# Kernel optimization log

Hardware: AMD Instinct MI355X
Metric: run time of the kernel (lower is better)

Reference implementation:

```python
import jax, jax.numpy as jnp
import numpy as np

N = 16384          # num nodes
E = 262144         # num edges (before self loops)
IN_DIM = 128
HID = 128
OUT = 2
TRIM = 0.1
MAX_DEG = 48       # padded max in-degree (incl. self loop); safe bound for Poisson(16)+1
BN_EPS = 1e-5


def _lin_params(key, fan_in, fan_out):
    kw, kb = jax.random.split(key)
    s = 1.0 / np.sqrt(fan_in)
    W = jax.random.uniform(kw, (fan_in, fan_out), jnp.float32, -s, s)
    b = jax.random.uniform(kb, (fan_out,), jnp.float32, -s, s)
    return W, b


def setup_inputs() -> dict:
    key = jax.random.key(0)
    ks = jax.random.split(key, 8)
    x = jax.random.normal(ks[0], (N, IN_DIM), jnp.float32)
    edge_index = jax.random.randint(ks[1], (2, E), 0, N, jnp.int32)
    Wl0, bl0 = _lin_params(ks[2], IN_DIM, HID)
    Wr0, br0 = _lin_params(ks[3], IN_DIM, HID)
    Wl1, bl1 = _lin_params(ks[4], HID, HID)
    Wr1, br1 = _lin_params(ks[5], HID, HID)
    Wl2, bl2 = _lin_params(ks[6], HID, OUT)
    Wr2, br2 = _lin_params(ks[7], HID, OUT)
    g0 = jnp.ones((HID,), jnp.float32); be0 = jnp.zeros((HID,), jnp.float32)
    g1 = jnp.ones((HID,), jnp.float32); be1 = jnp.zeros((HID,), jnp.float32)
    return dict(x=x, edge_index=edge_index,
                Wl0=Wl0, bl0=bl0, Wr0=Wr0, br0=br0, g0=g0, be0=be0,
                Wl1=Wl1, bl1=bl1, Wr1=Wr1, br1=br1, g1=g1, be1=be1,
                Wl2=Wl2, bl2=bl2, Wr2=Wr2, br2=br2)


def _forward(edge_index, x, Wl0, bl0, Wr0, br0, g0, be0,
             Wl1, bl1, Wr1, br1, g1, be1, Wl2, bl2, Wr2, br2):
    loops = jnp.arange(N, dtype=edge_index.dtype)
    row = jnp.concatenate([edge_index[0], loops])   # source nodes
    col = jnp.concatenate([edge_index[1], loops])   # destination nodes
    counts = jax.ops.segment_sum(jnp.ones_like(col), col, num_segments=N)  # in-degree, int
    deg = jnp.maximum(counts, 1).astype(x.dtype)
    norm = 1.0 / deg[col]                            # 1/deg(dst), per edge

    # Edge ordering grouped by destination node; rank = slot within the node's group.
    perm = jnp.argsort(col, stable=True)
    col_s = col[perm]
    starts = jnp.cumsum(counts) - counts
    rank = jnp.arange(col.shape[0], dtype=counts.dtype) - starts[col_s]
    node_id = jnp.where(rank < MAX_DEG, col_s, N)    # overflow slots -> OOB, dropped by scatter

    t = jnp.maximum(1, jnp.floor(counts.astype(jnp.float32) * TRIM).astype(counts.dtype))
    tcnt = counts - 2 * t
    pos = jnp.arange(MAX_DEG)[None, :]
    sel = (pos >= t[:, None]) & (pos < (counts - t)[:, None])   # [N, MAX_DEG]
    use_trim = (counts >= 5) & (tcnt > 0)
    inv_tcnt = 1.0 / jnp.maximum(tcnt, 1).astype(x.dtype)

    def trimmed_scatter(msg):
        # plain mean fallback
        mean = jax.ops.segment_sum(msg, col, num_segments=N) / deg[:, None]
        d = msg.shape[1]
        # padded per-node buffer; +inf pads sort to the end (never selected by `sel`)
        dense = jnp.full((N, MAX_DEG, d), jnp.inf, msg.dtype)
        dense = dense.at[node_id, rank].set(msg[perm], mode='drop')
        sdense = jnp.sort(dense, axis=1)             # per-feature sort within each node
        tmean = jnp.sum(jnp.where(sel[:, :, None], sdense, 0.0), axis=1) * inv_tcnt[:, None]
        return jnp.where(use_trim[:, None], tmean, mean)

    def conv(h, Wl, bl, Wr, br):
        msg = (h @ Wl + bl)[row] * norm[:, None]
        return trimmed_scatter(msg) + h @ Wr + br

    bn_scale = jnp.float32(1.0 / np.sqrt(1.0 + BN_EPS))  # eval-mode BN: running mean 0, var 1
    h = conv(x, Wl0, bl0, Wr0, br0)
    h = jax.nn.relu(h * bn_scale * g0 + be0)
    h = conv(h, Wl1, bl1, Wr1, br1)
    h = jax.nn.relu(h * bn_scale * g1 + be1)
    return conv(h, Wl2, bl2, Wr2, br2)


def reference(x, edge_index, Wl0, bl0, Wr0, br0, g0, be0,
              Wl1, bl1, Wr1, br1, g1, be1, Wl2, bl2, Wr2, br2):
    return _forward(edge_index, x, Wl0, bl0, Wr0, br0, g0, be0,
                    Wl1, bl1, Wr1, br1, g1, be1, Wl2, bl2, Wr2, br2)
```

## Files before the change

### kernel.cpp

```cpp
#include <hip/hip_runtime.h>
#include <hip/hip_fp16.h>
#include <math.h>

#define GN    16384
#define MAXD  48
#define BN_SCALE 0.9999950000374998f

typedef __attribute__((ext_vector_type(8))) short short8;
typedef __attribute__((ext_vector_type(4))) float f32x4;
typedef __attribute__((ext_vector_type(2))) float f32x2v;
typedef __attribute__((ext_vector_type(4))) float f32x4v;
typedef _Float16 __attribute__((ext_vector_type(2))) h2v;

__device__ inline short f2bf(float x) {
    unsigned u = __float_as_uint(x);
    return (short)((u + 0x7fffu + ((u >> 16) & 1u)) >> 16);
}
__device__ inline float bf2f(short s) {
    return __uint_as_float(((unsigned)(unsigned short)s) << 16);
}

struct F2 { float x, y; };
__device__ inline F2 f2min(F2 a, F2 b) { return {fminf(a.x, b.x), fminf(a.y, b.y)}; }
__device__ inline F2 f2max(F2 a, F2 b) { return {fmaxf(a.x, b.x), fmaxf(a.y, b.y)}; }

struct Trk {
    F2 tot, s0, s1, s2, s3, l0, l1, l2, l3;
};
__device__ inline void trk_init(Trk& T) {
    T.tot = {0.f, 0.f};
    T.s0 = T.s1 = T.s2 = T.s3 = { INFINITY,  INFINITY};
    T.l0 = T.l1 = T.l2 = T.l3 = {-INFINITY, -INFINITY};
}
__device__ inline void trk_push_light(Trk& T, F2 x, bool valid) {
    F2 xs = {valid ? x.x :  INFINITY, valid ? x.y :  INFINITY};
    F2 xl = {valid ? x.x : -INFINITY, valid ? x.y : -INFINITY};
    T.tot.x += valid ? x.x : 0.f;
    T.tot.y += valid ? x.y : 0.f;
    T.s0 = f2min(T.s0, xs);
    T.l0 = f2max(T.l0, xl);
}
__device__ inline void trk_push_full(Trk& T, F2 x, bool valid) {
    F2 a = {valid ? x.x :  INFINITY, valid ? x.y :  INFINITY};
    F2 b = {valid ? x.x : -INFINITY, valid ? x.y : -INFINITY};
    T.tot.x += valid ? x.x : 0.f;
    T.tot.y += valid ? x.y : 0.f;
    F2 t0 = f2min(T.s0, a); a = f2max(T.s0, a); T.s0 = t0;
    F2 t1 = f2min(T.s1, a); a = f2max(T.s1, a); T.s1 = t1;
    F2 t2 = f2min(T.s2, a); a = f2max(T.s2, a); T.s2 = t2;
    T.s3 = f2min(T.s3, a);
    F2 u0 = f2max(T.l0, b); b = f2min(T.l0, b); T.l0 = u0;
    F2 u1 = f2max(T.l1, b); b = f2min(T.l1, b); T.l1 = u1;
    F2 u2 = f2max(T.l2, b); b = f2min(T.l2, b); T.l2 = u2;
    T.l3 = f2max(T.l3, b);
}
__device__ inline F2 trk_finish(const Trk& T, int cnt) {
    int t = (int)floorf((float)cnt * 0.1f);
    if (t < 1) t = 1;
    int tcnt = cnt - 2 * t;
    bool use_trim = (cnt >= 5) && (tcnt > 0);
    float dd = (float)cnt;
    F2 res;
    if (use_trim) {
        int tt = min(t, 4);
        F2 bot = T.s0, top = T.l0;
        if (tt > 1) { bot.x += T.s1.x; bot.y += T.s1.y; top.x += T.l1.x; top.y += T.l1.y; }
        if (tt > 2) { bot.x += T.s2.x; bot.y += T.s2.y; top.x += T.l2.x; top.y += T.l2.y; }
        if (tt > 3) { bot.x += T.s3.x; bot.y += T.s3.y; top.x += T.l3.x; top.y += T.l3.y; }
        float inv = 1.0f / (dd * (float)tcnt);
        res.x = (T.tot.x - bot.x - top.x) * inv;
        res.y = (T.tot.y - bot.y - top.y) * inv;
    } else {
        float inv = 1.0f / (dd * dd);
        res.x = T.tot.x * inv;
        res.y = T.tot.y * inv;
    }
    return res;
}

__device__ inline F2 trim_core(const _Float16* __restrict__ HL,
                               const int* __restrict__ srow, int cnt, int d, int f2i)
{
    Trk T; trk_init(T);
    bool light = (cnt < 20);
    for (int i = 0; i < d; i += 8) {
        h2v b[8];
        #pragma unroll
        for (int k = 0; k < 8; ++k) {
            int ia = min(i + k, d - 1);
            b[k] = *reinterpret_cast<const h2v*>(HL + srow[ia] + f2i);
        }
        if (light) {
            #pragma unroll
            for (int k = 0; k < 8; ++k)
                trk_push_light(T, {(float)b[k][0], (float)b[k][1]}, i + k < d);
        } else {
            #pragma unroll
            for (int k = 0; k < 8; ++k)
                trk_push_full(T, {(float)b[k][0], (float)b[k][1]}, i + k < d);
        }
    }
    return trk_finish(T, cnt);
}

__global__ __launch_bounds__(256) void k_prep(
    int* __restrict__ fill,
    const float* __restrict__ Wl0, const float* __restrict__ Wr0,
    const float* __restrict__ Wl1, const float* __restrict__ Wr1,
    short* __restrict__ W5)
{
    int t = blockIdx.x * 256 + threadIdx.x;
    fill[t] = 0;

    int layer = t >> 13;
    int g     = t & 8191;
    int split = (g >> 12) & 1;
    int ks    = (g >> 10) & 3;
    int nt    = (g >> 6) & 15;
    int l     = g & 63;
    int q = l >> 4, r = l & 15;
    int n = nt * 16 + r;
    const float* W = (n < 128) ? (layer ? Wl1 : Wl0) : (layer ? Wr1 : Wr0);
    int ncol = n & 127;
    short8 o8;
    #pragma unroll
    for (int j = 0; j < 8; ++j) {
        int k = ks * 32 + (j >> 2) * 16 + q * 4 + (j & 3);
        float wv = W[k * 128 + ncol];
        short hi = f2bf(wv);
        o8[j] = split ? f2bf(wv - bf2f(hi)) : hi;
    }
    *reinterpret_cast<short8*>(W5 + ((size_t)layer * 8192 + g) * 8) = o8;
}

template<int NT>
__device__ inline void gemm_tile_t(const short8 Ahi[4], const short8 Alo[4],
                                   const short* __restrict__ W5,
                                   const float* __restrict__ bl,
                                   const float* __restrict__ br,
                                   _Float16* __restrict__ HL, float* __restrict__ HR,
                                   int tile, int half, int ntg0, int q, int r, int l)
{
    f32x4 acc[NT];
    #pragma unroll
    for (int nt = 0; nt < NT; ++nt) {
        int ntg = ntg0 + nt;
        float b = (ntg < 8) ? bl[ntg * 16 + r] : br[(ntg - 8) * 16 + r];
        acc[nt] = (f32x4){b, b, b, b};
    }
    #pragma unroll
    for (int ks = 0; ks < 4; ++ks) {
        #pragma unroll
        for (int nt = 0; nt < NT; ++nt) {
            int ntg = ntg0 + nt;
            short8 Bhi = *reinterpret_cast<const short8*>(
                W5 + ((size_t)(ks * 16 + ntg) * 64 + l) * 8);
            short8 Blo = *reinterpret_cast<const short8*>(
                W5 + ((size_t)((4 + ks) * 16 + ntg) * 64 + l) * 8);
            acc[nt] = __builtin_amdgcn_mfma_f32_16x16x32_bf16(Ahi[ks], Bhi, acc[nt], 0, 0, 0);
            acc[nt] = __builtin_amdgcn_mfma_f32_16x16x32_bf16(Ahi[ks], Blo, acc[nt], 0, 0, 0);
            acc[nt] = __builtin_amdgcn_mfma_f32_16x16x32_bf16(Alo[ks], Bhi, acc[nt], 0, 0, 0);
        }
    }
    const int rb = tile * 32 + half * 16 + 4 * q;
    #pragma unroll
    for (int nt = 0; nt < NT; ++nt) {
        int ntg = ntg0 + nt;
        if (ntg < 8) {
            int c = ntg * 16 + r;
            #pragma unroll
            for (int j = 0; j < 4; ++j)
                HL[(size_t)(rb + j) * 128 + c] = (_Float16)acc[nt][j];
        } else {
            int c = (ntg - 8) * 16 + r;
            #pragma unroll
            for (int j = 0; j < 4; ++j)
                __builtin_nontemporal_store(acc[nt][j], &HR[(size_t)(rb + j) * 128 + c]);
        }
    }
}

__global__ __launch_bounds__(512, 4) void k_fused0(
    const float* __restrict__ X, const int* __restrict__ ei, int E,
    int* __restrict__ adj, int* __restrict__ fill,
    const short* __restrict__ W5,
    const float* __restrict__ bl, const float* __restrict__ br,
    _Float16* __restrict__ HL, float* __restrict__ HR)
{
    const int tid = threadIdx.x;
    if (blockIdx.x >= 512) {
        const int* src = ei;
        const int* dst = ei + E;
        int g0 = (blockIdx.x - 512) * 512 + tid;
        for (int i = g0; i < E + GN; i += 64 * 512) {
            int s, dv;
            if (i < E) { s = src[i]; dv = dst[i]; }
            else       { s = i - E;  dv = i - E; }
            int slot = atomicAdd(&fill[dv], 1);
            if (slot < MAXD) adj[dv * MAXD + slot] = s;
        }
        return;
    }
    const int w = tid >> 6, l = tid & 63;
    const int q = l >> 4, r = l & 15;
    const int half = w & 1, quarter = w >> 1;
    const int rowA = blockIdx.x * 32 + half * 16 + r;

    short8 Ahi[4], Alo[4];
    const f32x4v* xp = reinterpret_cast<const f32x4v*>(X + (size_t)rowA * 128);
    #pragma unroll
    for (int h = 0; h < 8; ++h) {
        f32x4v v = __builtin_nontemporal_load(xp + h * 4 + q);
        float xv[4] = {v.x, v.y, v.z, v.w};
        int ks = h >> 1, hk = h & 1;
        #pragma unroll
        for (int j = 0; j < 4; ++j) {
            short hi = f2bf(xv[j]);
            Ahi[ks][hk * 4 + j] = hi;
            Alo[ks][hk * 4 + j] = f2bf(xv[j] - bf2f(hi));
        }
    }
    gemm_tile_t<4>(Ahi, Alo, W5, bl, br, HL, HR, blockIdx.x, half, quarter * 4, q, r, l);
}

__global__ __launch_bounds__(512, 4) void k_fused1(
    const _Float16* __restrict__ HL0, const float* __restrict__ HR0,
    const int* __restrict__ adj, const int* __restrict__ fill,
    const float* __restrict__ g, const float* __restrict__ be,
    const short* __restrict__ W5,
    const float* __restrict__ bl, const float* __restrict__ br,
    _Float16* __restrict__ HL1, float* __restrict__ HR1)
{
    __shared__ float hbs[32][132];
    __shared__ int sadj[8][2][MAXD];
    const int tid = threadIdx.x, w = tid >> 6, l = tid & 63;
    const int f2i = l * 2;
    const int v0 = blockIdx.x * 32;
    const float gs0 = BN_SCALE * g[f2i], gs1 = BN_SCALE * g[f2i + 1];
    const float be0 = be[f2i], be1 = be[f2i + 1];

    for (int p = 0; p < 2; ++p) {
        const int vA = v0 + w * 4 + p * 2;
        const int vB = vA + 1;
        const int cA = fill[vA], cB = fill[vB];
        const int dA = min(cA, MAXD), dB = min(cB, MAXD);
        if (l < dA) sadj[w][0][l] = adj[vA * MAXD + l] * 128;
        if (l < dB) sadj[w][1][l] = adj[vB * MAXD + l] * 128;

        Trk TA, TB;
        trk_init(TA); trk_init(TB);
        const bool light = (cA < 20) && (cB < 20);
        const int dmax = max(dA, dB);
        for (int i = 0; i < dmax; i += 8) {
            h2v bA[8], bB[8];
            #pragma unroll
            for (int k = 0; k < 8; ++k) {
                int iaA = min(i + k, dA - 1);
                int iaB = min(i + k, dB - 1);
                bA[k] = *reinterpret_cast<const h2v*>(HL0 + sadj[w][0][iaA] + f2i);
                bB[k] = *reinterpret_cast<const h2v*>(HL0 + sadj[w][1][iaB] + f2i);
            }
            if (light) {
                #pragma unroll
                for (int k = 0; k < 8; ++k) {
                    trk_push_light(TA, {(float)bA[k][0], (float)bA[k][1]}, i + k < dA);
                    trk_push_light(TB, {(float)bB[k][0], (float)bB[k][1]}, i + k < dB);
                }
            } else {
                #pragma unroll
                for (int k = 0; k < 8; ++k) {
                    trk_push_full(TA, {(float)bA[k][0], (float)bA[k][1]}, i + k < dA);
                    trk_push_full(TB, {(float)bB[k][0], (float)bB[k][1]}, i + k < dB);
                }
            }
        }
        F2 rA = trk_finish(TA, cA);
        F2 rB = trk_finish(TB, cB);
        const f32x2v hrA = __builtin_nontemporal_load(
            reinterpret_cast<const f32x2v*>(HR0 + (size_t)vA * 128 + f2i));
        const f32x2v hrB = __builtin_nontemporal_load(
            reinterpret_cast<const f32x2v*>(HR0 + (size_t)vB * 128 + f2i));
        hbs[w * 4 + p * 2][f2i]         = fmaxf((rA.x + hrA.x) * gs0 + be0, 0.f);
        hbs[w * 4 + p * 2][f2i + 1]     = fmaxf((rA.y + hrA.y) * gs1 + be1, 0.f);
        hbs[w * 4 + p * 2 + 1][f2i]     = fmaxf((rB.x + hrB.x) * gs0 + be0, 0.f);
        hbs[w * 4 + p * 2 + 1][f2i + 1] = fmaxf((rB.y + hrB.y) * gs1 + be1, 0.f);
    }
    __syncthreads();

    const int q = l >> 4, r = l & 15;
    const int half = w & 1, quarter = w >> 1;
    const int m = half * 16 + r;
    short8 Ahi[4], Alo[4];
    #pragma unroll
    for (int h = 0; h < 8; ++h) {
        float4 vv = *reinterpret_cast<const float4*>(&hbs[m][h * 16 + 4 * q]);
        float xv[4] = {vv.x, vv.y, vv.z, vv.w};
        int ks = h >> 1, hk = h & 1;
        #pragma unroll
        for (int j = 0; j < 4; ++j) {
            short hi = f2bf(xv[j]);
            Ahi[ks][hk * 4 + j] = hi;
            Alo[ks][hk * 4 + j] = f2bf(xv[j] - bf2f(hi));
        }
    }
    gemm_tile_t<4>(Ahi, Alo, W5, bl, br, HL1, HR1, blockIdx.x, half, quarter * 4, q, r, l);
}

__global__ __launch_bounds__(256) void k_fused2(
    const _Float16* __restrict__ HL1, const float* __restrict__ HR1,
    const int* __restrict__ adj, const int* __restrict__ fill,
    const float* __restrict__ g, const float* __restrict__ be,
    const float* __restrict__ Wl2, const float* __restrict__ bl2,
    const float* __restrict__ Wr2, const float* __restrict__ br2,
    float* __restrict__ hl2, float* __restrict__ hr2)
{
    __shared__ int sadj[4][MAXD];
    const int tid = threadIdx.x, w = tid >> 6, l = tid & 63;
    const int f2i = l * 2;
    const int v = blockIdx.x * 4 + w;
    const int cnt = fill[v];
    const int d = min(cnt, MAXD);
    if (l < d) sadj[w][l] = adj[v * MAXD + l] * 128;
    F2 res = trim_core(HL1, sadj[w], cnt, d, f2i);
    const f32x2v hrv = __builtin_nontemporal_load(
        reinterpret_cast<const f32x2v*>(HR1 + (size_t)v * 128 + f2i));
    float h0 = fmaxf((res.x + hrv.x) * (BN_SCALE * g[f2i])     + be[f2i],     0.f);
    float h1 = fmaxf((res.y + hrv.y) * (BN_SCALE * g[f2i + 1]) + be[f2i + 1], 0.f);

    float4 wl = *reinterpret_cast<const float4*>(Wl2 + l * 4);
    float4 wr = *reinterpret_cast<const float4*>(Wr2 + l * 4);
    float p0 = h0 * wl.x + h1 * wl.z;
    float p1 = h0 * wl.y + h1 * wl.w;
    float p2 = h0 * wr.x + h1 * wr.z;
    float p3 = h0 * wr.y + h1 * wr.w;
    #pragma unroll
    for (int off = 1; off < 64; off <<= 1) {
        p0 += __shfl_xor(p0, off);
        p1 += __shfl_xor(p1, off);
        p2 += __shfl_xor(p2, off);
        p3 += __shfl_xor(p3, off);
    }
    if (l == 0) {
        hl2[v * 2 + 0] = p0 + bl2[0];
        hl2[v * 2 + 1] = p1 + bl2[1];
        hr2[v * 2 + 0] = p2 + br2[0];
        hr2[v * 2 + 1] = p3 + br2[1];
    }
}

__global__ __launch_bounds__(256) void k_agg_out(
    const float* __restrict__ hl2, const float* __restrict__ hr2,
    const int* __restrict__ adj, const int* __restrict__ fill,
    float* __restrict__ out)
{
    int idx = blockIdx.x * 256 + threadIdx.x;
    int v = idx >> 1, j = idx & 1;
    int cnt = fill[v];
    int d = min(cnt, MAXD);
    const int* ap = adj + v * MAXD;

    float total = 0.f;
    float s0 = INFINITY, s1 = INFINITY, s2 = INFINITY, s3 = INFINITY;
    float l0 = -INFINITY, l1 = -INFINITY, l2 = -INFINITY, l3 = -INFINITY;
    for (int i = 0; i < d; i += 8) {
        float b[8];
        bool val[8];
        #pragma unroll
        for (int k = 0; k < 8; ++k) {
            int ia = min(i + k, d - 1);
            b[k] = hl2[ap[ia] * 2 + j];
            val[k] = (i + k) < d;
        }
        #pragma unroll
        for (int k = 0; k < 8; ++k) {
            float xs = val[k] ? b[k] :  INFINITY;
            float xl = val[k] ? b[k] : -INFINITY;
            total += val[k] ? b[k] : 0.f;
            float a = xs;
            float t0 = fminf(s0, a); a = fmaxf(s0, a); s0 = t0;
            float t1 = fminf(s1, a); a = fmaxf(s1, a); s1 = t1;
            float t2 = fminf(s2, a); a = fmaxf(s2, a); s2 = t2;
            s3 = fminf(s3, a);
            float bb = xl;
            float u0 = fmaxf(l0, bb); bb = fminf(l0, bb); l0 = u0;
            float u1 = fmaxf(l1, bb); bb = fminf(l1, bb); l1 = u1;
            float u2 = fmaxf(l2, bb); bb = fminf(l2, bb); l2 = u2;
            l3 = fmaxf(l3, bb);
        }
    }

    int t = (int)floorf((float)cnt * 0.1f);
    if (t < 1) t = 1;
    int tcnt = cnt - 2 * t;
    bool use_trim = (cnt >= 5) && (tcnt > 0);
    float dd = (float)cnt;
    float res;
    if (use_trim) {
        int tt = min(t, 4);
        float bot = s0, top = l0;
        if (tt > 1) { bot += s1; top += l1; }
        if (tt > 2) { bot += s2; top += l2; }
        if (tt > 3) { bot += s3; top += l3; }
        res = (total - bot - top) / (dd * (float)tcnt);
    } else {
        res = total / (dd * dd);
    }
    out[idx] = res + hr2[idx];
}

extern "C" void kernel_launch(void* const* d_in, const int* in_sizes, int n_in,
                              void* d_out, int out_size, void* d_ws, size_t ws_size,
                              hipStream_t stream)
{
    const float* x   = (const float*)d_in[0];
    const int*   ei  = (const int*)d_in[1];
    const int    E   = in_sizes[1] / 2;
    const float* Wl0 = (const float*)d_in[2];
    const float* bl0 = (const float*)d_in[3];
    const float* Wr0 = (const float*)d_in[4];
    const float* br0 = (const float*)d_in[5];
    const float* g0  = (const float*)d_in[6];
    const float* be0 = (const float*)d_in[7];
    const float* Wl1 = (const float*)d_in[8];
    const float* bl1 = (const float*)d_in[9];
    const float* Wr1 = (const float*)d_in[10];
    const float* br1 = (const float*)d_in[11];
    const float* g1  = (const float*)d_in[12];
    const float* be1 = (const float*)d_in[13];
    const float* Wl2 = (const float*)d_in[14];
    const float* bl2 = (const float*)d_in[15];
    const float* Wr2 = (const float*)d_in[16];
    const float* br2 = (const float*)d_in[17];
    float* out = (float*)d_out;

    char* w = (char*)d_ws;
    int*      adj  = (int*)w;       w += (size_t)GN * MAXD * 4;
    int*      fill = (int*)w;       w += (size_t)GN * 4;
    _Float16* HL0  = (_Float16*)w;  w += (size_t)GN * 128 * 2;
    float*    HR0  = (float*)w;     w += (size_t)GN * 128 * 4;
    _Float16* HL1  = (_Float16*)w;  w += (size_t)GN * 128 * 2;
    float*    HR1  = (float*)w;     w += (size_t)GN * 128 * 4;
    short*    W5   = (short*)w;     w += (size_t)2 * 8192 * 16;
    float*    hl2  = (float*)w;     w += (size_t)GN * 2 * 4;
    float*    hr2  = (float*)w;     w += (size_t)GN * 2 * 4;

    k_prep  <<<GN / 256, 256, 0, stream>>>(fill, Wl0, Wr0, Wl1, Wr1, W5);
    k_fused0<<<576, 512, 0, stream>>>(x, ei, E, adj, fill, W5, bl0, br0, HL0, HR0);
    k_fused1<<<GN / 32, 512, 0, stream>>>(HL0, HR0, adj, fill, g0, be0,
                                          W5 + (size_t)8192 * 8, bl1, br1, HL1, HR1);
    k_fused2<<<GN / 4, 256, 0, stream>>>(HL1, HR1, adj, fill, g1, be1,
                                         Wl2, bl2, Wr2, br2, hl2, hr2);
    k_agg_out<<<GN * 2 / 256, 256, 0, stream>>>(hl2, hr2, adj, fill, out);
}
```

Baseline: 193.7 us.

## Keep adjacency in registers via readlane and specialize trim tracker depth by degree

Each wave now loads the node's adjacency list into one register per lane and broadcasts neighbor offsets with readlane, replacing the shared-memory staging. Layer 1 now processes one node at a time (four per wave) instead of interleaving two. The trimmed-mean tracker gains a middle mode that keeps two extremes for degrees 20-29, and full 8-wide chunks skip the validity masking, leaving masking only on the tail chunk. Nontemporal loads and stores are also replaced by plain accesses. The risks are lower memory-level parallelism from dropping the two-node interleave and extra code size from the three specialized paths.

Measured after the change: 177.1 us. 8.6% less time.

```diff
diff --git a/kernel.cpp b/kernel.cpp
--- a/kernel.cpp
+++ b/kernel.cpp
@@ -8,8 +8,6 @@
 
 typedef __attribute__((ext_vector_type(8))) short short8;
 typedef __attribute__((ext_vector_type(4))) float f32x4;
-typedef __attribute__((ext_vector_type(2))) float f32x2v;
-typedef __attribute__((ext_vector_type(4))) float f32x4v;
 typedef _Float16 __attribute__((ext_vector_type(2))) h2v;
 
 __device__ inline short f2bf(float x) {
@@ -32,23 +30,28 @@
     T.s0 = T.s1 = T.s2 = T.s3 = { INFINITY,  INFINITY};
     T.l0 = T.l1 = T.l2 = T.l3 = {-INFINITY, -INFINITY};
 }
-__device__ inline void trk_push_light(Trk& T, F2 x, bool valid) {
-    F2 xs = {valid ? x.x :  INFINITY, valid ? x.y :  INFINITY};
-    F2 xl = {valid ? x.x : -INFINITY, valid ? x.y : -INFINITY};
-    T.tot.x += valid ? x.x : 0.f;
-    T.tot.y += valid ? x.y : 0.f;
-    T.s0 = f2min(T.s0, xs);
-    T.l0 = f2max(T.l0, xl);
-}
-__device__ inline void trk_push_full(Trk& T, F2 x, bool valid) {
-    F2 a = {valid ? x.x :  INFINITY, valid ? x.y :  INFINITY};
-    F2 b = {valid ? x.x : -INFINITY, valid ? x.y : -INFINITY};
-    T.tot.x += valid ? x.x : 0.f;
-    T.tot.y += valid ? x.y : 0.f;
+__device__ inline void push1(Trk& T, F2 x) {
+    T.tot.x += x.x; T.tot.y += x.y;
+    T.s0 = f2min(T.s0, x);
+    T.l0 = f2max(T.l0, x);
+}
+__device__ inline void push2(Trk& T, F2 x) {
+    T.tot.x += x.x; T.tot.y += x.y;
+    F2 a = x;
+    F2 t0 = f2min(T.s0, a); a = f2max(T.s0, a); T.s0 = t0;
+    T.s1 = f2min(T.s1, a);
+    F2 b = x;
+    F2 u0 = f2max(T.l0, b); b = f2min(T.l0, b); T.l0 = u0;
+    T.l1 = f2max(T.l1, b);
+}
+__device__ inline void push4(Trk& T, F2 x) {
+    T.tot.x += x.x; T.tot.y += x.y;
+    F2 a = x;
     F2 t0 = f2min(T.s0, a); a = f2max(T.s0, a); T.s0 = t0;
     F2 t1 = f2min(T.s1, a); a = f2max(T.s1, a); T.s1 = t1;
     F2 t2 = f2min(T.s2, a); a = f2max(T.s2, a); T.s2 = t2;
     T.s3 = f2min(T.s3, a);
+    F2 b = x;
     F2 u0 = f2max(T.l0, b); b = f2min(T.l0, b); T.l0 = u0;
     F2 u1 = f2max(T.l1, b); b = f2min(T.l1, b); T.l1 = u1;
     F2 u2 = f2max(T.l2, b); b = f2min(T.l2, b); T.l2 = u2;
@@ -78,26 +81,69 @@
     return res;
 }
 
-__device__ inline F2 trim_core(const _Float16* __restrict__ HL,
-                               const int* __restrict__ srow, int cnt, int d, int f2i)
-{
+__device__ inline F2 trim_core_reg(const _Float16* __restrict__ HL,
+                                   int adjb, int cnt, int d, int f2i2)
+{
+    const char* HLc = (const char*)HL;
     Trk T; trk_init(T);
-    bool light = (cnt < 20);
-    for (int i = 0; i < d; i += 8) {
+    const int mode = (cnt < 20) ? 0 : ((cnt < 30) ? 1 : 2);
+
+    int i = 0;
+    for (; i + 8 <= d; i += 8) {
+        h2v b[8];
+        #pragma unroll
+        for (int k = 0; k < 8; ++k) {
+            int sofs = __builtin_amdgcn_readlane(adjb, i + k);
+            b[k] = *reinterpret_cast<const h2v*>(HLc + sofs + f2i2);
+        }
+        if (mode == 0) {
+            #pragma unroll
+            for (int k = 0; k < 8; ++k) push1(T, {(float)b[k][0], (float)b[k][1]});
+        } else if (mode == 1) {
+            #pragma unroll
+            for (int k = 0; k < 8; ++k) push2(T, {(float)b[k][0], (float)b[k][1]});
+        } else {
+            #pragma unroll
+            for (int k = 0; k < 8; ++k) push4(T, {(float)b[k][0], (float)b[k][1]});
+        }
+    }
+    if (i < d) {
         h2v b[8];
         #pragma unroll
         for (int k = 0; k < 8; ++k) {
             int ia = min(i + k, d - 1);
-            b[k] = *reinterpret_cast<const h2v*>(HL + srow[ia] + f2i);
-        }
-        if (light) {
-            #pragma unroll
-            for (int k = 0; k < 8; ++k)
-                trk_push_light(T, {(float)b[k][0], (float)b[k][1]}, i + k < d);
-        } else {
-            #pragma unroll
-            for (int k = 0; k < 8; ++k)
-                trk_push_full(T, {(float)b[k][0], (float)b[k][1]}, i + k < d);
+            int sofs = __builtin_amdgcn_readlane(adjb, ia);
+            b[k] = *reinterpret_cast<const h2v*>(HLc + sofs + f2i2);
+        }
+        #pragma unroll
+        for (int k = 0; k < 8; ++k) {
+            bool vld = (i + k) < d;
+            F2 x = {vld ? (float)b[k][0] : 0.f, vld ? (float)b[k][1] : 0.f};
+            F2 xs = {vld ? x.x :  INFINITY, vld ? x.y :  INFINITY};
+            F2 xl = {vld ? x.x : -INFINITY, vld ? x.y : -INFINITY};
+            T.tot.x += x.x; T.tot.y += x.y;
+            if (mode == 0) {
+                T.s0 = f2min(T.s0, xs);
+                T.l0 = f2max(T.l0, xl);
+            } else if (mode == 1) {
+                F2 a = xs;
+                F2 t0 = f2min(T.s0, a); a = f2max(T.s0, a); T.s0 = t0;
+                T.s1 = f2min(T.s1, a);
+                F2 bb = xl;
+                F2 u0 = f2max(T.l0, bb); bb = f2min(T.l0, bb); T.l0 = u0;
+                T.l1 = f2max(T.l1, bb);
+            } else {
+                F2 a = xs;
+                F2 t0 = f2min(T.s0, a); a = f2max(T.s0, a); T.s0 = t0;
+                F2 t1 = f2min(T.s1, a); a = f2max(T.s1, a); T.s1 = t1;
+                F2 t2 = f2min(T.s2, a); a = f2max(T.s2, a); T.s2 = t2;
+                T.s3 = f2min(T.s3, a);
+                F2 bb = xl;
+                F2 u0 = f2max(T.l0, bb); bb = f2min(T.l0, bb); T.l0 = u0;
+                F2 u1 = f2max(T.l1, bb); bb = f2min(T.l1, bb); T.l1 = u1;
+                F2 u2 = f2max(T.l2, bb); bb = f2min(T.l2, bb); T.l2 = u2;
+                T.l3 = f2max(T.l3, bb);
+            }
         }
     }
     return trk_finish(T, cnt);
@@ -175,7 +221,7 @@
             int c = (ntg - 8) * 16 + r;
             #pragma unroll
             for (int j = 0; j < 4; ++j)
-                __builtin_nontemporal_store(acc[nt][j], &HR[(size_t)(rb + j) * 128 + c]);
+                HR[(size_t)(rb + j) * 128 + c] = acc[nt][j];
         }
     }
 }
@@ -207,10 +253,10 @@
     const int rowA = blockIdx.x * 32 + half * 16 + r;
 
     short8 Ahi[4], Alo[4];
-    const f32x4v* xp = reinterpret_cast<const f32x4v*>(X + (size_t)rowA * 128);
+    const float4* xp = reinterpret_cast<const float4*>(X + (size_t)rowA * 128);
     #pragma unroll
     for (int h = 0; h < 8; ++h) {
-        f32x4v v = __builtin_nontemporal_load(xp + h * 4 + q);
+        float4 v = xp[h * 4 + q];
         float xv[4] = {v.x, v.y, v.z, v.w};
         int ks = h >> 1, hk = h & 1;
         #pragma unroll
@@ -232,58 +278,23 @@
     _Float16* __restrict__ HL1, float* __restrict__ HR1)
 {
     __shared__ float hbs[32][132];
-    __shared__ int sadj[8][2][MAXD];
     const int tid = threadIdx.x, w = tid >> 6, l = tid & 63;
     const int f2i = l * 2;
+    const int f2i2 = f2i * 2;
     const int v0 = blockIdx.x * 32;
     const float gs0 = BN_SCALE * g[f2i], gs1 = BN_SCALE * g[f2i + 1];
     const float be0 = be[f2i], be1 = be[f2i + 1];
 
-    for (int p = 0; p < 2; ++p) {
-        const int vA = v0 + w * 4 + p * 2;
-        const int vB = vA + 1;
-        const int cA = fill[vA], cB = fill[vB];
-        const int dA = min(cA, MAXD), dB = min(cB, MAXD);
-        if (l < dA) sadj[w][0][l] = adj[vA * MAXD + l] * 128;
-        if (l < dB) sadj[w][1][l] = adj[vB * MAXD + l] * 128;
-
-        Trk TA, TB;
-        trk_init(TA); trk_init(TB);
-        const bool light = (cA < 20) && (cB < 20);
-        const int dmax = max(dA, dB);
-        for (int i = 0; i < dmax; i += 8) {
-            h2v bA[8], bB[8];
-            #pragma unroll
-            for (int k = 0; k < 8; ++k) {
-                int iaA = min(i + k, dA - 1);
-                int iaB = min(i + k, dB - 1);
-                bA[k] = *reinterpret_cast<const h2v*>(HL0 + sadj[w][0][iaA] + f2i);
-                bB[k] = *reinterpret_cast<const h2v*>(HL0 + sadj[w][1][iaB] + f2i);
-            }
-            if (light) {
-                #pragma unroll
-                for (int k = 0; k < 8; ++k) {
-                    trk_push_light(TA, {(float)bA[k][0], (float)bA[k][1]}, i + k < dA);
-                    trk_push_light(TB, {(float)bB[k][0], (float)bB[k][1]}, i + k < dB);
-                }
-            } else {
-                #pragma unroll
-                for (int k = 0; k < 8; ++k) {
-                    trk_push_full(TA, {(float)bA[k][0], (float)bA[k][1]}, i + k < dA);
-                    trk_push_full(TB, {(float)bB[k][0], (float)bB[k][1]}, i + k < dB);
-                }
-            }
-        }
-        F2 rA = trk_finish(TA, cA);
-        F2 rB = trk_finish(TB, cB);
-        const f32x2v hrA = __builtin_nontemporal_load(
-            reinterpret_cast<const f32x2v*>(HR0 + (size_t)vA * 128 + f2i));
-        const f32x2v hrB = __builtin_nontemporal_load(
-            reinterpret_cast<const f32x2v*>(HR0 + (size_t)vB * 128 + f2i));
-        hbs[w * 4 + p * 2][f2i]         = fmaxf((rA.x + hrA.x) * gs0 + be0, 0.f);
-        hbs[w * 4 + p * 2][f2i + 1]     = fmaxf((rA.y + hrA.y) * gs1 + be1, 0.f);
-        hbs[w * 4 + p * 2 + 1][f2i]     = fmaxf((rB.x + hrB.x) * gs0 + be0, 0.f);
-        hbs[w * 4 + p * 2 + 1][f2i + 1] = fmaxf((rB.y + hrB.y) * gs1 + be1, 0.f);
+    #pragma unroll
+    for (int s = 0; s < 4; ++s) {
+        const int v = v0 + w * 4 + s;
+        const int cnt = fill[v];
+        const int d = min(cnt, MAXD);
+        const int adjb = adj[v * MAXD + min(l, d - 1)] << 8;
+        F2 res = trim_core_reg(HL0, adjb, cnt, d, f2i2);
+        const float2 hrv = *reinterpret_cast<const float2*>(HR0 + (size_t)v * 128 + f2i);
+        hbs[w * 4 + s][f2i]     = fmaxf((res.x + hrv.x) * gs0 + be0, 0.f);
+        hbs[w * 4 + s][f2i + 1] = fmaxf((res.y + hrv.y) * gs1 + be1, 0.f);
     }
     __syncthreads();
 
@@ -314,16 +325,15 @@
     const float* __restrict__ Wr2, const float* __restrict__ br2,
     float* __restrict__ hl2, float* __restrict__ hr2)
 {
-    __shared__ int sadj[4][MAXD];
     const int tid = threadIdx.x, w = tid >> 6, l = tid & 63;
     const int f2i = l * 2;
+    const int f2i2 = f2i * 2;
     const int v = blockIdx.x * 4 + w;
     const int cnt = fill[v];
     const int d = min(cnt, MAXD);
-    if (l < d) sadj[w][l] = adj[v * MAXD + l] * 128;
-    F2 res = trim_core(HL1, sadj[w], cnt, d, f2i);
-    const f32x2v hrv = __builtin_nontemporal_load(
-        reinterpret_cast<const f32x2v*>(HR1 + (size_t)v * 128 + f2i));
+    const int adjb = adj[v * MAXD + min(l, d - 1)] << 8;
+    F2 res = trim_core_reg(HL1, adjb, cnt, d, f2i2);
+    const float2 hrv = *reinterpret_cast<const float2*>(HR1 + (size_t)v * 128 + f2i);
     float h0 = fmaxf((res.x + hrv.x) * (BN_SCALE * g[f2i])     + be[f2i],     0.f);
     float h1 = fmaxf((res.y + hrv.y) * (BN_SCALE * g[f2i + 1]) + be[f2i + 1], 0.f);
 
```
